# Optimization experiments

Hardware: AMD Instinct MI355X
Metric: run time of the kernel (lower is better)

## Reference

```python
import jax, jax.numpy as jnp
import numpy as np

EMBED, HIDDEN, VOCAB = 256, 512, 32000
B, T = 16, 63  # captions length; total steps per item = T+1


def setup_inputs() -> dict:
    key = jax.random.key(0)
    ks = jax.random.split(key, 9)
    s = 0.05
    return {
        "features": jax.random.normal(ks[0], (B, EMBED), jnp.float32),
        "captions": jax.random.randint(ks[1], (B, T), 0, VOCAB, jnp.int32),
        "emb": jax.random.normal(ks[2], (VOCAB, EMBED), jnp.float32) * s,
        "W_ih": jax.random.normal(ks[3], (4 * HIDDEN, EMBED), jnp.float32) * s,
        "W_hh": jax.random.normal(ks[4], (4 * HIDDEN, HIDDEN), jnp.float32) * s,
        "b_ih": jax.random.normal(ks[5], (4 * HIDDEN,), jnp.float32) * s,
        "b_hh": jax.random.normal(ks[6], (4 * HIDDEN,), jnp.float32) * s,
        "W_out": jax.random.normal(ks[7], (VOCAB, HIDDEN), jnp.float32) * s,
        "b_out": jax.random.normal(ks[8], (VOCAB,), jnp.float32) * s,
    }


def reference(features, captions, emb, W_ih, W_hh, b_ih, b_hh, W_out, b_out):
    H = W_hh.shape[1]
    embeds = emb[captions]  # [B, T, E]
    # inputs = cat(features.unsqueeze(1), embeds, dim=1) -> [B, T+1, E]
    inputs = jnp.concatenate([features[:, None, :], embeds], axis=1)
    # The torch loop threads self.hidden across batch items -> one long
    # sequential LSTM over B*(T+1) steps starting from zero state.
    xs = inputs.reshape(-1, inputs.shape[-1])  # [B*(T+1), E]
    # precompute input projections for all steps (one big GEMM)
    x_proj = xs @ W_ih.T + b_ih + b_hh  # [S, 4H]

    def cell(carry, xp):
        h, c = carry
        gates = xp + h @ W_hh.T  # [4H]
        i, f, g, o = jnp.split(gates, 4)
        i = jax.nn.sigmoid(i)
        f = jax.nn.sigmoid(f)
        g = jnp.tanh(g)
        o = jax.nn.sigmoid(o)
        c = f * c + i * g
        h = o * jnp.tanh(c)
        return (h, c), h

    h0 = jnp.zeros((H,), xs.dtype)
    c0 = jnp.zeros((H,), xs.dtype)
    _, hs = jax.lax.scan(cell, (h0, c0), x_proj)  # [S, H]
    logits = hs @ W_out.T + b_out  # [S, V]
    probs = jax.nn.softmax(logits, axis=-1)
    return probs.reshape(inputs.shape[0], inputs.shape[1], -1)  # [B, T+1, V]
```

## Files before the change

### kernel.cpp

```cpp
#include <hip/hip_runtime.h>
#include <cstdint>
#include <cstddef>

#define EMBED  256
#define HIDDEN 512
#define VOCAB  32000
#define BATCH  16
#define TCAP   63
#define STEPS  1024
#define GROWS  2048

#define WS_HBUF  0
#define WS_HS32  8192
#define WS_HSBF  2105344
#define WS_WB    3153920
#define WS_XPOFF (24u * 1024u * 1024u)
#define WS_NEED  36708352ull
#define WB_HEAD_ELEMS 12582912

typedef __bf16 bf16x8 __attribute__((ext_vector_type(8)));
typedef float  f32x4  __attribute__((ext_vector_type(4)));
typedef unsigned int u32x4v __attribute__((ext_vector_type(4)));

__device__ __forceinline__ float sigmoid_f(float x) {
    return 1.0f / (1.0f + __expf(-x));
}
__device__ __forceinline__ float tanh_f(float x) {
    float a = fabsf(x);
    float e = __expf(-2.0f * a);
    float r = (1.0f - e) / (1.0f + e);
    return copysignf(r, x);
}
__device__ __forceinline__ float sel4(float a0, float a1, float a2, float a3, int j) {
    float lo = (j & 1) ? a1 : a0;
    float hi = (j & 1) ? a3 : a2;
    return (j & 2) ? hi : lo;
}
__device__ __forceinline__ unsigned short f2bf_u16(float f) {
    union { float f; unsigned u; } v; v.f = f;
    unsigned r = v.u + 0x7fffu + ((v.u >> 16) & 1u);
    return (unsigned short)(r >> 16);
}

__global__ __launch_bounds__(256) void xproj_kernel(
    const float* __restrict__ features,
    const int*   __restrict__ captions,
    const float* __restrict__ emb,
    const float* __restrict__ W_ih,
    const float* __restrict__ b_ih,
    const float* __restrict__ b_hh,
    float* __restrict__ xp)
{
    __shared__ float As[64][65];
    __shared__ float Bs[64][65];
    const int tid = threadIdx.x;
    const int tx = tid & 15, ty = tid >> 4;
    const int r0 = blockIdx.x * 64;
    const int s0 = blockIdx.y * 64;
    float accv[4][4] = {};

    for (int k0 = 0; k0 < EMBED; k0 += 64) {
#pragma unroll
        for (int i = 0; i < 4; ++i) {
            const int idx = tid + i * 256;
            const int row = idx >> 4, q = idx & 15;
            const int s = s0 + row, sb = s >> 6, st = s & 63;
            const float* xr = (st == 0)
                ? (features + (size_t)sb * EMBED)
                : (emb + (size_t)captions[sb * TCAP + st - 1] * EMBED);
            const float4 a = *(const float4*)(xr + k0 + q * 4);
            As[row][q * 4 + 0] = a.x; As[row][q * 4 + 1] = a.y;
            As[row][q * 4 + 2] = a.z; As[row][q * 4 + 3] = a.w;
            const float4 b = *(const float4*)(W_ih + (size_t)(r0 + row) * EMBED + k0 + q * 4);
            Bs[row][q * 4 + 0] = b.x; Bs[row][q * 4 + 1] = b.y;
            Bs[row][q * 4 + 2] = b.z; Bs[row][q * 4 + 3] = b.w;
        }
        __syncthreads();
#pragma unroll 16
        for (int kk = 0; kk < 64; ++kk) {
            float av[4], bv[4];
#pragma unroll
            for (int i = 0; i < 4; ++i) av[i] = As[ty * 4 + i][kk];
#pragma unroll
            for (int j = 0; j < 4; ++j) bv[j] = Bs[tx * 4 + j][kk];
#pragma unroll
            for (int i = 0; i < 4; ++i)
#pragma unroll
                for (int j = 0; j < 4; ++j)
                    accv[i][j] = fmaf(av[i], bv[j], accv[i][j]);
        }
        __syncthreads();
    }
#pragma unroll
    for (int j = 0; j < 4; ++j) {
        const int r = r0 + tx * 4 + j;
        const float bb = b_ih[r] + b_hh[r];
#pragma unroll
        for (int i = 0; i < 4; ++i)
            xp[(size_t)(s0 + ty * 4 + i) * GROWS + r] = accv[i][j] + bb;
    }
}

__global__ __launch_bounds__(256, 1) void lstm_scan_kernel(
    const float* __restrict__ W_hh,
    const float* __restrict__ xp,
    unsigned long long* __restrict__ hbuf,
    float* __restrict__ hs32,
    __bf16* __restrict__ hsbf,
    const float* __restrict__ W_out,
    unsigned short* __restrict__ Wb,
    const int wbf)
{
    const int tid = threadIdx.x;

    if (blockIdx.x >= 32) {
        if (!wbf) return;
        const int cb = blockIdx.x - 32;
        const int stride = 224 * 256 * 4;
        for (int i = (cb * 256 + tid) * 4; i < WB_HEAD_ELEMS; i += stride) {
            const float4 v = *(const float4*)(W_out + i);
            ushort4 o;
            o.x = f2bf_u16(v.x); o.y = f2bf_u16(v.y);
            o.z = f2bf_u16(v.z); o.w = f2bf_u16(v.w);
            *(ushort4*)(Wb + i) = o;
        }
        return;
    }

    const int rg  = tid >> 6;
    const int kc  = tid & 63;
    const int w   = blockIdx.x * 4 + rg;
    const int j0  = w * 4;

    __shared__ float hlds[2][HIDDEN];

    const int t_own  = ((kc & 1) << 1) | ((kc >> 1) & 1);
    const int jj_own = (((kc >> 2) & 1) << 1) | ((kc >> 3) & 1);
    const int row_own = t_own * HIDDEN + j0 + jj_own;

    float Whh[4][4][8];
#pragma unroll
    for (int t = 0; t < 4; ++t) {
#pragma unroll
        for (int jj = 0; jj < 4; ++jj) {
            const int row = t * HIDDEN + j0 + jj;
            const float4* ph = (const float4*)(W_hh + (size_t)row * HIDDEN + kc * 8);
            const float4 h0 = ph[0], h1 = ph[1];
            Whh[t][jj][0] = h0.x; Whh[t][jj][1] = h0.y; Whh[t][jj][2] = h0.z; Whh[t][jj][3] = h0.w;
            Whh[t][jj][4] = h1.x; Whh[t][jj][5] = h1.y; Whh[t][jj][6] = h1.z; Whh[t][jj][7] = h1.w;
        }
    }

    float c_state = 0.0f;
    float xpv_next = xp[row_own];
    const int qi = rg * 128 + kc * 2;

    for (int s = 0; s < STEPS; ++s) {
        const int p = s & 1;
        const unsigned expect = (unsigned)s;
        const float xpv = xpv_next;

        const int sn = (s + 1 < STEPS) ? (s + 1) : (STEPS - 1);
        xpv_next = xp[(size_t)sn * GROWS + row_own];

        const unsigned long long fa =
            (unsigned long long)(hbuf + (size_t)p * HIDDEN + qi);
        unsigned d0, d1;
        for (;;) {
            u32x4v v;
            asm volatile("global_load_dwordx4 %0, %1, off sc0 sc1\n\t"
                         "s_waitcnt vmcnt(0)"
                         : "=&v"(v) : "v"(fa) : "memory");
            if (__all((int)((v.y == expect) & (v.w == expect)))) {
                d0 = v.x; d1 = v.z; break;
            }
        }
        hlds[p][qi]     = __uint_as_float(d0);
        hlds[p][qi + 1] = __uint_as_float(d1);
        __syncthreads();

        float hreg[8];
        {
            const float4 a = *(const float4*)&hlds[p][kc * 8];
            const float4 b = *(const float4*)&hlds[p][kc * 8 + 4];
            hreg[0] = a.x; hreg[1] = a.y; hreg[2] = a.z; hreg[3] = a.w;
            hreg[4] = b.x; hreg[5] = b.y; hreg[6] = b.z; hreg[7] = b.w;
        }

        float acc[16];
#pragma unroll
        for (int t = 0; t < 4; ++t) {
#pragma unroll
            for (int jj = 0; jj < 4; ++jj) {
                float a = Whh[t][jj][0] * hreg[0];
#pragma unroll
                for (int kk = 1; kk < 8; ++kk)
                    a = fmaf(Whh[t][jj][kk], hreg[kk], a);
                acc[t * 4 + jj] = a;
            }
        }

#pragma unroll
        for (int i = 0; i < 8; ++i) {
            const float send = (kc & 1) ? acc[i] : acc[i + 8];
            const float keep = (kc & 1) ? acc[i + 8] : acc[i];
            acc[i] = keep + __shfl_xor(send, 1, 64);
        }
#pragma unroll
        for (int i = 0; i < 4; ++i) {
            const float send = (kc & 2) ? acc[i] : acc[i + 4];
            const float keep = (kc & 2) ? acc[i + 4] : acc[i];
            acc[i] = keep + __shfl_xor(send, 2, 64);
        }
#pragma unroll
        for (int i = 0; i < 2; ++i) {
            const float send = (kc & 4) ? acc[i] : acc[i + 2];
            const float keep = (kc & 4) ? acc[i + 2] : acc[i];
            acc[i] = keep + __shfl_xor(send, 4, 64);
        }
        {
            const float send = (kc & 8) ? acc[0] : acc[1];
            const float keep = (kc & 8) ? acc[1] : acc[0];
            acc[0] = keep + __shfl_xor(send, 8, 64);
        }
        float a = acc[0];
        a += __shfl_xor(a, 16, 64);
        a += __shfl_xor(a, 32, 64);
        a += xpv;

        const float g00 = a;
        const float g01 = __shfl_xor(a, 1, 64);
        const float g10 = __shfl_xor(a, 2, 64);
        const float g11 = __shfl_xor(g01, 2, 64);
        float gi = sel4(g00, g10, g01, g11, t_own);
        float gf = sel4(g00, g10, g01, g11, t_own ^ 1);
        float gg = sel4(g00, g10, g01, g11, t_own ^ 2);
        float go = sel4(g00, g10, g01, g11, t_own ^ 3);

        gi = sigmoid_f(gi);
        gf = sigmoid_f(gf);
        gg = tanh_f(gg);
        go = sigmoid_f(go);
        c_state = gf * c_state + gi * gg;
        const float hnew = go * tanh_f(c_state);

        if ((kc & 0x33) == 0) {
            const int j = j0 + jj_own;
            const unsigned long long pack =
                ((unsigned long long)(unsigned)(s + 1) << 32) |
                (unsigned long long)__float_as_uint(hnew);
            __hip_atomic_store(hbuf + (size_t)((s + 1) & 1) * HIDDEN + j, pack,
                               __ATOMIC_RELAXED, __HIP_MEMORY_SCOPE_AGENT);
            if (wbf) hsbf[(size_t)s * HIDDEN + j] = (__bf16)hnew;
            else     hs32[(size_t)s * HIDDEN + j] = hnew;
        }
    }
}

__global__ __launch_bounds__(256) void convert_tail_kernel(
    const float* __restrict__ W, unsigned short* __restrict__ Wb,
    int lo, int n)
{
    const int stride = gridDim.x * blockDim.x * 4;
    for (int i = lo + (blockIdx.x * blockDim.x + threadIdx.x) * 4; i < n; i += stride) {
        const float4 v = *(const float4*)(W + i);
        ushort4 o;
        o.x = f2bf_u16(v.x); o.y = f2bf_u16(v.y);
        o.z = f2bf_u16(v.z); o.w = f2bf_u16(v.w);
        *(ushort4*)(Wb + i) = o;
    }
}

__global__ __launch_bounds__(256) void logits_mfma_kernel(
    const __bf16* __restrict__ A,
    const __bf16* __restrict__ B,
    const float* __restrict__ b_out,
    float* __restrict__ out)
{
    __shared__ char AsR[16384];
    __shared__ char BsR[16384];
    const int tid  = threadIdx.x;
    const int lane = tid & 63;
    const int wave = tid >> 6;
    const int wm = (wave >> 1) * 64;
    const int wn = (wave & 1) * 64;
    const int n0 = blockIdx.x * 128;
    const int m0 = blockIdx.y * 128;

    f32x4 acc[4][4] = {};

    for (int k0 = 0; k0 < HIDDEN; k0 += 64) {
        if (k0) __syncthreads();
#pragma unroll
        for (int i = 0; i < 4; ++i) {
            const int o   = (tid + i * 256) << 4;
            const int row = o >> 7;
            const int cb  = o & 127;
            const int sc  = cb ^ ((row & 7) << 4);
            const bf16x8 av = *(const bf16x8*)(A + (size_t)(m0 + row) * HIDDEN + k0 + (cb >> 1));
            const bf16x8 bv = *(const bf16x8*)(B + (size_t)(n0 + row) * HIDDEN + k0 + (cb >> 1));
            *(bf16x8*)(AsR + row * 128 + sc) = av;
            *(bf16x8*)(BsR + row * 128 + sc) = bv;
        }
        __syncthreads();
#pragma unroll
        for (int ks = 0; ks < 2; ++ks) {
            const int kb = ks * 64 + ((lane >> 4) << 4);
            bf16x8 af[4], bfr[4];
#pragma unroll
            for (int mi = 0; mi < 4; ++mi) {
                const int r = wm + mi * 16 + (lane & 15);
                af[mi] = *(const bf16x8*)(AsR + r * 128 + (kb ^ ((r & 7) << 4)));
            }
#pragma unroll
            for (int ni = 0; ni < 4; ++ni) {
                const int r = wn + ni * 16 + (lane & 15);
                bfr[ni] = *(const bf16x8*)(BsR + r * 128 + (kb ^ ((r & 7) << 4)));
            }
#pragma unroll
            for (int mi = 0; mi < 4; ++mi)
#pragma unroll
                for (int ni = 0; ni < 4; ++ni)
                    acc[mi][ni] = __builtin_amdgcn_mfma_f32_16x16x32_bf16(
                        af[mi], bfr[ni], acc[mi][ni], 0, 0, 0);
        }
    }

#pragma unroll
    for (int ni = 0; ni < 4; ++ni) {
        const int col = n0 + wn + ni * 16 + (lane & 15);
        const float bo = b_out[col];
#pragma unroll
        for (int mi = 0; mi < 4; ++mi) {
            const int r0 = m0 + wm + mi * 16 + ((lane >> 4) << 2);
#pragma unroll
            for (int qq = 0; qq < 4; ++qq)
                out[(size_t)(r0 + qq) * VOCAB + col] = acc[mi][ni][qq] + bo;
        }
    }
}

__global__ __launch_bounds__(256) void logits_kernel(
    const float* __restrict__ hs,
    const float* __restrict__ W_out,
    const float* __restrict__ b_out,
    float* __restrict__ out)
{
    __shared__ float As[64][65];
    __shared__ float Bs[64][65];
    const int tid = threadIdx.x;
    const int tx = tid & 15, ty = tid >> 4;
    const int v0 = blockIdx.x * 64;
    const int s0 = blockIdx.y * 64;
    float accv[4][4] = {};

    for (int k0 = 0; k0 < HIDDEN; k0 += 64) {
#pragma unroll
        for (int i = 0; i < 4; ++i) {
            const int idx = tid + i * 256;
            const int r = idx >> 4, q = idx & 15;
            const float4 a = *(const float4*)(hs + (size_t)(s0 + r) * HIDDEN + k0 + q * 4);
            As[r][q * 4 + 0] = a.x; As[r][q * 4 + 1] = a.y;
            As[r][q * 4 + 2] = a.z; As[r][q * 4 + 3] = a.w;
            const float4 b = *(const float4*)(W_out + (size_t)(v0 + r) * HIDDEN + k0 + q * 4);
            Bs[r][q * 4 + 0] = b.x; Bs[r][q * 4 + 1] = b.y;
            Bs[r][q * 4 + 2] = b.z; Bs[r][q * 4 + 3] = b.w;
        }
        __syncthreads();
#pragma unroll 16
        for (int kk = 0; kk < 64; ++kk) {
            float av[4], bv[4];
#pragma unroll
            for (int i = 0; i < 4; ++i) av[i] = As[ty * 4 + i][kk];
#pragma unroll
            for (int j = 0; j < 4; ++j) bv[j] = Bs[tx * 4 + j][kk];
#pragma unroll
            for (int i = 0; i < 4; ++i)
#pragma unroll
                for (int j = 0; j < 4; ++j)
                    accv[i][j] = fmaf(av[i], bv[j], accv[i][j]);
        }
        __syncthreads();
    }
#pragma unroll
    for (int i = 0; i < 4; ++i) {
        const int s = s0 + ty * 4 + i;
#pragma unroll
        for (int j = 0; j < 4; ++j) {
            const int v = v0 + tx * 4 + j;
            out[(size_t)s * VOCAB + v] = accv[i][j] + b_out[v];
        }
    }
}

__global__ __launch_bounds__(1024, 1) void softmax_kernel(float* __restrict__ out)
{
    __shared__ float redm[16];
    __shared__ float redl[16];
    const int row = blockIdx.x;
    float* p = out + (size_t)row * VOCAB;
    const int tid  = threadIdx.x;
    const int lane = tid & 63, wv = tid >> 6;

    float r[32];
    float m = -3.402823466e38f, l = 0.0f;
#pragma unroll
    for (int c = 0; c < 8; ++c) {
        const int i = c * 4096 + tid * 4;
        if (i < VOCAB) {
            const float4 v = *(const float4*)(p + i);
            r[c * 4 + 0] = v.x; r[c * 4 + 1] = v.y;
            r[c * 4 + 2] = v.z; r[c * 4 + 3] = v.w;
            const float m4 = fmaxf(fmaxf(v.x, v.y), fmaxf(v.z, v.w));
            const float mn = fmaxf(m, m4);
            l = l * __expf(m - mn)
              + __expf(v.x - mn) + __expf(v.y - mn)
              + __expf(v.z - mn) + __expf(v.w - mn);
            m = mn;
        }
    }

#pragma unroll
    for (int d = 1; d < 64; d <<= 1) {
        const float mo = __shfl_xor(m, d, 64);
        const float lo = __shfl_xor(l, d, 64);
        const float mn = fmaxf(m, mo);
        l = l * __expf(m - mn) + lo * __expf(mo - mn);
        m = mn;
    }
    if (lane == 0) { redm[wv] = m; redl[wv] = l; }
    __syncthreads();

    m = redm[0]; l = redl[0];
#pragma unroll
    for (int i2 = 1; i2 < 16; ++i2) {
        const float mo = redm[i2], lo = redl[i2];
        const float mn = fmaxf(m, mo);
        l = l * __expf(m - mn) + lo * __expf(mo - mn);
        m = mn;
    }
    const float inv = 1.0f / l;

#pragma unroll
    for (int c = 0; c < 8; ++c) {
        const int i = c * 4096 + tid * 4;
        if (i < VOCAB) {
            float4 o;
            o.x = __expf(r[c * 4 + 0] - m) * inv;
            o.y = __expf(r[c * 4 + 1] - m) * inv;
            o.z = __expf(r[c * 4 + 2] - m) * inv;
            o.w = __expf(r[c * 4 + 3] - m) * inv;
            *(float4*)(p + i) = o;
        }
    }
}

extern "C" void kernel_launch(void* const* d_in, const int* in_sizes, int n_in,
                              void* d_out, int out_size, void* d_ws, size_t ws_size,
                              hipStream_t stream)
{
    const float* features = (const float*)d_in[0];
    const int*   captions = (const int*)d_in[1];
    const float* emb      = (const float*)d_in[2];
    const float* W_ih     = (const float*)d_in[3];
    const float* W_hh     = (const float*)d_in[4];
    const float* b_ih     = (const float*)d_in[5];
    const float* b_hh     = (const float*)d_in[6];
    const float* W_out    = (const float*)d_in[7];
    const float* b_out    = (const float*)d_in[8];
    float* out = (float*)d_out;

    char* ws = (char*)d_ws;
    unsigned long long* hbuf = (unsigned long long*)(ws + WS_HBUF);
    float*              hs32 = (float*)(ws + WS_HS32);
    __bf16*             hsbf = (__bf16*)(ws + WS_HSBF);
    __bf16*             Wb   = (__bf16*)(ws + WS_WB);
    const bool mfma_ok = ws_size >= WS_NEED;
    float* xpb = mfma_ok ? (float*)(ws + WS_WB + WS_XPOFF) : (float*)(ws + WS_WB);

    hipMemsetAsync(d_ws, 0, 8192, stream);

    xproj_kernel<<<dim3(GROWS / 64, STEPS / 64), 256, 0, stream>>>(
        features, captions, emb, W_ih, b_ih, b_hh, xpb);

    lstm_scan_kernel<<<mfma_ok ? 256 : 32, 256, 0, stream>>>(
        W_hh, xpb, hbuf, hs32, hsbf,
        W_out, (unsigned short*)Wb, mfma_ok ? 1 : 0);

    if (mfma_ok) {
        convert_tail_kernel<<<512, 256, 0, stream>>>(
            W_out, (unsigned short*)Wb, WB_HEAD_ELEMS, VOCAB * HIDDEN);
        logits_mfma_kernel<<<dim3(VOCAB / 128, STEPS / 128), 256, 0, stream>>>(
            hsbf, Wb, b_out, out);
    } else {
        logits_kernel<<<dim3(VOCAB / 64, STEPS / 64), 256, 0, stream>>>(
            hs32, W_out, b_out, out);
    }
    softmax_kernel<<<STEPS, 1024, 0, stream>>>(out);
}
```

Baseline: 1.915 ms.

## Add helper polling wavefronts racing compute waves to fetch hidden state

```diff
diff --git a/kernel.cpp b/kernel.cpp
--- a/kernel.cpp
+++ b/kernel.cpp
@@ -101,7 +101,7 @@
     }
 }
 
-__global__ __launch_bounds__(256, 1) void lstm_scan_kernel(
+__global__ __launch_bounds__(512, 1) void lstm_scan_kernel(
     const float* __restrict__ W_hh,
     const float* __restrict__ xp,
     unsigned long long* __restrict__ hbuf,
@@ -116,8 +116,8 @@
     if (blockIdx.x >= 32) {
         if (!wbf) return;
         const int cb = blockIdx.x - 32;
-        const int stride = 224 * 256 * 4;
-        for (int i = (cb * 256 + tid) * 4; i < WB_HEAD_ELEMS; i += stride) {
+        const int stride = 224 * 512 * 4;
+        for (int i = (cb * 512 + tid) * 4; i < WB_HEAD_ELEMS; i += stride) {
             const float4 v = *(const float4*)(W_out + i);
             ushort4 o;
             o.x = f2bf_u16(v.x); o.y = f2bf_u16(v.y);
@@ -129,10 +129,42 @@
 
     const int rg  = tid >> 6;
     const int kc  = tid & 63;
-    const int w   = blockIdx.x * 4 + rg;
-    const int j0  = w * 4;
+    const int q   = rg & 3;
+    const int qi  = q * 128 + kc * 2;
 
     __shared__ float hlds[2][HIDDEN];
+    __shared__ unsigned flg[2][4];
+
+    if (tid < 8) ((volatile unsigned*)&flg[0][0])[tid] = 0xffffffffu;
+    __syncthreads();
+
+    if (rg >= 4) {
+        for (int s = 0; s < STEPS; ++s) {
+            const int p = s & 1;
+            const unsigned expect = (unsigned)s;
+            volatile unsigned* f = (volatile unsigned*)&flg[p][q];
+            const unsigned long long fa =
+                (unsigned long long)(hbuf + (size_t)p * HIDDEN + qi);
+            for (;;) {
+                u32x4v v;
+                asm volatile("global_load_dwordx4 %0, %1, off sc0 sc1\n\t"
+                             "s_waitcnt vmcnt(0)"
+                             : "=&v"(v) : "v"(fa) : "memory");
+                if (__all((int)((v.y == expect) & (v.w == expect)))) {
+                    hlds[p][qi]     = __uint_as_float(v.x);
+                    hlds[p][qi + 1] = __uint_as_float(v.z);
+                    if (kc == 0) *f = expect;
+                    break;
+                }
+                if (*f == expect) break;
+            }
+            __syncthreads();
+        }
+        return;
+    }
+
+    const int w  = blockIdx.x * 4 + rg;
+    const int j0 = w * 4;
 
     const int t_own  = ((kc & 1) << 1) | ((kc >> 1) & 1);
     const int jj_own = (((kc >> 2) & 1) << 1) | ((kc >> 3) & 1);
@@ -153,7 +185,6 @@
 
     float c_state = 0.0f;
     float xpv_next = xp[row_own];
-    const int qi = rg * 128 + kc * 2;
 
     for (int s = 0; s < STEPS; ++s) {
         const int p = s & 1;
@@ -163,20 +194,24 @@
         const int sn = (s + 1 < STEPS) ? (s + 1) : (STEPS - 1);
         xpv_next = xp[(size_t)sn * GROWS + row_own];
 
-        const unsigned long long fa =
-            (unsigned long long)(hbuf + (size_t)p * HIDDEN + qi);
-        unsigned d0, d1;
-        for (;;) {
-            u32x4v v;
-            asm volatile("global_load_dwordx4 %0, %1, off sc0 sc1\n\t"
-                         "s_waitcnt vmcnt(0)"
-                         : "=&v"(v) : "v"(fa) : "memory");
-            if (__all((int)((v.y == expect) & (v.w == expect)))) {
-                d0 = v.x; d1 = v.z; break;
+        {
+            volatile unsigned* f = (volatile unsigned*)&flg[p][q];
+            const unsigned long long fa =
+                (unsigned long long)(hbuf + (size_t)p * HIDDEN + qi);
+            for (;;) {
+                if (*f == expect) break;
+                u32x4v v;
+                asm volatile("global_load_dwordx4 %0, %1, off sc0 sc1\n\t"
+                             "s_waitcnt vmcnt(0)"
+                             : "=&v"(v) : "v"(fa) : "memory");
+                if (__all((int)((v.y == expect) & (v.w == expect)))) {
+                    hlds[p][qi]     = __uint_as_float(v.x);
+                    hlds[p][qi + 1] = __uint_as_float(v.z);
+                    if (kc == 0) *f = expect;
+                    break;
+                }
             }
         }
-        hlds[p][qi]     = __uint_as_float(d0);
-        hlds[p][qi + 1] = __uint_as_float(d1);
         __syncthreads();
 
         float hreg[8];
@@ -483,7 +518,7 @@
     xproj_kernel<<<dim3(GROWS / 64, STEPS / 64), 256, 0, stream>>>(
         features, captions, emb, W_ih, b_ih, b_hh, xpb);
 
-    lstm_scan_kernel<<<mfma_ok ? 256 : 32, 256, 0, stream>>>(
+    lstm_scan_kernel<<<mfma_ok ? 256 : 32, 512, 0, stream>>>(
         W_hh, xpb, hbuf, hs32, hsbf,
         W_out, (unsigned short*)Wb, mfma_ok ? 1 : 0);
 
```

Result: slower. 2.232 ms (+16.5%).
